# Performance work log

Hardware: AMD Instinct MI355X
Metric: run time of the kernel (lower is better)

The kernel has to match this reference:

```python
import jax, jax.numpy as jnp
import numpy as np

F = 1024
H = 16
DH = F // H  # 64
MLP = 4096
EPS = 1e-5


def layernorm(x, g, b):
    mu = x.mean(-1, keepdims=True)
    var = ((x - mu) ** 2).mean(-1, keepdims=True)
    return (x - mu) * jax.lax.rsqrt(var + EPS) * g + b


def softmax_off_by_one(a):
    e = jnp.exp(a - a.max(-1, keepdims=True))
    return e / (1.0 + e.sum(-1, keepdims=True))


def setup_inputs() -> dict:
    key = jax.random.key(0)
    ks = jax.random.split(key, 12)
    s = 0.02
    return {
        "x": jax.random.normal(ks[0], (2, 2048, F), jnp.float32),
        "ln1_g": jnp.ones((F,), jnp.float32),
        "ln1_b": jnp.zeros((F,), jnp.float32),
        "Wq": jax.random.normal(ks[1], (F, F), jnp.float32) * s,
        "bq": jnp.zeros((F,), jnp.float32),
        "Wk": jax.random.normal(ks[2], (F, F), jnp.float32) * s,
        "bk": jnp.zeros((F,), jnp.float32),
        "Wv": jax.random.normal(ks[3], (F, F), jnp.float32) * s,
        "bv": jnp.zeros((F,), jnp.float32),
        "Wo": jax.random.normal(ks[4], (F, F), jnp.float32) * s,
        "bo": jnp.zeros((F,), jnp.float32),
        "slim": jnp.ones((H,), jnp.float32),
        "ln2_g": jnp.ones((F,), jnp.float32),
        "ln2_b": jnp.zeros((F,), jnp.float32),
        "W1": jax.random.normal(ks[5], (F, MLP), jnp.float32) * s,
        "b1": jnp.zeros((MLP,), jnp.float32),
        "W2": jax.random.normal(ks[6], (MLP, F), jnp.float32) * s,
        "b2": jnp.zeros((F,), jnp.float32),
    }


def reference(x, ln1_g, ln1_b, Wq, bq, Wk, bk, Wv, bv, Wo, bo, slim,
              ln2_g, ln2_b, W1, b1, W2, b2):
    b, n, f = x.shape
    h = layernorm(x, ln1_g, ln1_b)
    # project and split heads: [b, H, n, DH]
    q = (h @ Wq + bq).reshape(b, n, H, DH).transpose(0, 2, 1, 3)
    k = (h @ Wk + bk).reshape(b, n, H, DH).transpose(0, 2, 1, 3)
    v = (h @ Wv + bv).reshape(b, n, H, DH).transpose(0, 2, 1, 3)
    att = jnp.einsum('bhid,bhjd->bhij', q, k) / (DH ** 0.5)
    probs = softmax_off_by_one(att)  # off-by-one softmax
    probs = probs * slim[None, :, None, None]  # slimming after softmax
    attn = jnp.einsum('bhij,bhjd->bihd', probs, v).reshape(b, n, F)
    out = attn @ Wo + bo + x  # residual 1
    h2 = layernorm(out, ln2_g, ln2_b)
    m = jax.nn.gelu(h2 @ W1 + b1, approximate=False)
    m = jax.nn.gelu(m @ W2 + b2, approximate=False)
    return m + out  # residual 2
```

## Files before the change

### kernel.cpp

```cpp
#include <hip/hip_runtime.h>
#include <hip/hip_bf16.h>

typedef __hip_bfloat16 bf16;
typedef short bf16x8 __attribute__((ext_vector_type(8)));
typedef float f32x4 __attribute__((ext_vector_type(4)));

__device__ __forceinline__ float gelu_f(float x) {
  return 0.5f * x * (1.f + erff(x * 0.70710678118654752f));
}

__device__ __forceinline__ unsigned short f2bfu(float f) {
  bf16 h = __float2bfloat16(f);
  unsigned short u;
  __builtin_memcpy(&u, &h, 2);
  return u;
}

__device__ __forceinline__ void load16_lds(const bf16* g, bf16* l) {
  __builtin_amdgcn_global_load_lds(
      (const __attribute__((address_space(1))) unsigned int*)g,
      (__attribute__((address_space(3))) unsigned int*)l, 16, 0, 0);
}

__global__ __launch_bounds__(256) void transpose_cast(
    const float* __restrict__ src, bf16* __restrict__ dst, int R, int C) {
  __shared__ float tile[32][33];
  int tx = threadIdx.x & 31, ty = threadIdx.x >> 5;
  int r0 = blockIdx.y * 32, c0 = blockIdx.x * 32;
  #pragma unroll
  for (int i = ty; i < 32; i += 8)
    tile[i][tx] = src[(size_t)(r0 + i) * C + (c0 + tx)];
  __syncthreads();
  #pragma unroll
  for (int i = ty; i < 32; i += 8)
    dst[(size_t)(c0 + i) * R + (r0 + tx)] = __float2bfloat16(tile[tx][i]);
}

__global__ __launch_bounds__(256) void ln_kernel(
    const float* __restrict__ x, const float* __restrict__ g,
    const float* __restrict__ b, bf16* __restrict__ y) {
  int row = blockIdx.x;
  int t = threadIdx.x;
  const float4* xr = (const float4*)(x + (size_t)row * 1024);
  float4 v = xr[t];
  float s = v.x + v.y + v.z + v.w;
  float ss = v.x * v.x + v.y * v.y + v.z * v.z + v.w * v.w;
  #pragma unroll
  for (int off = 32; off >= 1; off >>= 1) {
    s += __shfl_xor(s, off);
    ss += __shfl_xor(ss, off);
  }
  __shared__ float red[8];
  int wv = t >> 6;
  if ((t & 63) == 0) { red[wv] = s; red[4 + wv] = ss; }
  __syncthreads();
  float S = red[0] + red[1] + red[2] + red[3];
  float SS = red[4] + red[5] + red[6] + red[7];
  float mu = S * (1.f / 1024.f);
  float var = SS * (1.f / 1024.f) - mu * mu;
  float inv = rsqrtf(var + 1e-5f);
  float4 gv = ((const float4*)g)[t];
  float4 bv = ((const float4*)b)[t];
  ushort4 o;
  o.x = f2bfu((v.x - mu) * inv * gv.x + bv.x);
  o.y = f2bfu((v.y - mu) * inv * gv.y + bv.y);
  o.z = f2bfu((v.z - mu) * inv * gv.z + bv.z);
  o.w = f2bfu((v.w - mu) * inv * gv.w + bv.w);
  ((ushort4*)(y + (size_t)row * 1024))[t] = o;
}

template <int EPI>
__global__ __launch_bounds__(256) void gemm_bf16(
    const bf16* __restrict__ A, const bf16* __restrict__ Bt,
    const float* __restrict__ bias0, const float* __restrict__ bias1,
    const float* __restrict__ bias2, const float* __restrict__ resid,
    void* __restrict__ C0, void* __restrict__ C1, void* __restrict__ C2,
    int M, int N, int K) {
  __shared__ __align__(16) bf16 As[2][128 * 32];
  __shared__ __align__(16) bf16 Bs[2][128 * 32];
  const int t = threadIdx.x, lane = t & 63, w = t >> 6;
  const int wm = (w >> 1) * 64, wn = (w & 1) * 64;
  const int m0 = blockIdx.y * 128, n0 = blockIdx.x * 128;

  const int koff = (EPI == 6) ? (int)blockIdx.z * 1024 : 0;
  const int kc_len = (EPI == 6) ? 1024 : K;

  const int srow = lane >> 2;
  const int sgrp = lane & 3;
  f32x4 acc[4][4] = {};

  const bf16* Abase = A + (size_t)m0 * K + koff;
  const bf16* Bbase = Bt + (size_t)n0 * K + koff;

  auto stage = [&](int buf, int kt) {
    #pragma unroll
    for (int c = 0; c < 2; ++c) {
      int row = w * 32 + c * 16 + srow;
      int sw = (row & 3) ^ ((row >> 2) & 3);
      int gg = sgrp ^ sw;
      const bf16* ga = Abase + (size_t)row * K + kt + gg * 8;
      const bf16* gb = Bbase + (size_t)row * K + kt + gg * 8;
      load16_lds(ga, &As[buf][(w * 32 + c * 16) * 32]);
      load16_lds(gb, &Bs[buf][(w * 32 + c * 16) * 32]);
    }
  };

  const int q8 = (((lane >> 4) ^ (lane & 3) ^ ((lane >> 2) & 3))) * 8;
  const int fr = lane & 15;

  const int nk = kc_len >> 5;
  stage(0, 0);
  for (int i = 0; i < nk; ++i) {
    const int cur = i & 1;
    __syncthreads();
    if (i + 1 < nk) stage(cur ^ 1, (i + 1) << 5);
    bf16x8 af[4], bfr[4];
    #pragma unroll
    for (int mc = 0; mc < 4; ++mc)
      af[mc] = *(const bf16x8*)&As[cur][(wm + mc * 16 + fr) * 32 + q8];
    #pragma unroll
    for (int nc = 0; nc < 4; ++nc)
      bfr[nc] = *(const bf16x8*)&Bs[cur][(wn + nc * 16 + fr) * 32 + q8];
    #pragma unroll
    for (int mc = 0; mc < 4; ++mc)
      #pragma unroll
      for (int nc = 0; nc < 4; ++nc)
        acc[mc][nc] = __builtin_amdgcn_mfma_f32_16x16x32_bf16(
            af[mc], bfr[nc], acc[mc][nc], 0, 0, 0);
  }

  if constexpr (EPI == 0) {
    const int which = n0 >> 10;
    const float* bp = which == 0 ? bias0 : which == 1 ? bias1 : bias2;
    bf16* qk = (bf16*)(which == 0 ? C0 : C1);
    const float qscale = 0.18033688011112042f;
    #pragma unroll
    for (int mc = 0; mc < 4; ++mc) {
      #pragma unroll
      for (int reg = 0; reg < 4; ++reg) {
        int m = m0 + wm + mc * 16 + ((lane >> 4) << 2) + reg;
        int b = m >> 11, tok = m & 2047;
        #pragma unroll
        for (int nc = 0; nc < 4; ++nc) {
          int n = n0 + wn + nc * 16 + (lane & 15);
          int nn = n & 1023, hh = nn >> 6, d = n & 63;
          float val = acc[mc][nc][reg] + bp[nn];
          if (which == 2)
            ((bf16*)C2)[(size_t)((b * 16 + hh) * 64 + d) * 2048 + tok] =
                __float2bfloat16(val);
          else if (which == 0)
            qk[(size_t)((b * 16 + hh) * 2048 + tok) * 64 + d] =
                __float2bfloat16(val * qscale);
          else
            qk[(size_t)((b * 16 + hh) * 2048 + tok) * 64 + d] =
                __float2bfloat16(val);
        }
      }
    }
  } else if constexpr (EPI == 6) {
    bf16* pout = (bf16*)C0 + (size_t)blockIdx.z * M * N;
    #pragma unroll
    for (int mc = 0; mc < 4; ++mc) {
      #pragma unroll
      for (int reg = 0; reg < 4; ++reg) {
        int m = m0 + wm + mc * 16 + ((lane >> 4) << 2) + reg;
        #pragma unroll
        for (int nc = 0; nc < 4; ++nc) {
          int n = n0 + wn + nc * 16 + (lane & 15);
          pout[(size_t)m * N + n] = __float2bfloat16(acc[mc][nc][reg]);
        }
      }
    }
  } else {
    #pragma unroll
    for (int mc = 0; mc < 4; ++mc) {
      #pragma unroll
      for (int reg = 0; reg < 4; ++reg) {
        int m = m0 + wm + mc * 16 + ((lane >> 4) << 2) + reg;
        #pragma unroll
        for (int nc = 0; nc < 4; ++nc) {
          int n = n0 + wn + nc * 16 + (lane & 15);
          float val = acc[mc][nc][reg] + bias0[n];
          size_t idx = (size_t)m * N + n;
          if constexpr (EPI == 3) {
            ((float*)C0)[idx] = val + resid[idx];
          } else if constexpr (EPI == 4) {
            ((bf16*)C0)[idx] = __float2bfloat16(gelu_f(val));
          } else {
            ((float*)C0)[idx] = gelu_f(val) + resid[idx];
          }
        }
      }
    }
  }
}

__global__ __launch_bounds__(256) void reduce_mlp2(
    const bf16* __restrict__ part, const float* __restrict__ b2,
    const float* __restrict__ out1, float* __restrict__ out) {
  const int row = blockIdx.x, t = threadIdx.x;
  const size_t base = (size_t)row * 1024 + t * 4;
  float sum[4] = {0.f, 0.f, 0.f, 0.f};
  #pragma unroll
  for (int kc = 0; kc < 4; ++kc) {
    ushort4 u = *(const ushort4*)(part + (size_t)kc * 4096 * 1024 + base);
    unsigned short us[4] = {u.x, u.y, u.z, u.w};
    #pragma unroll
    for (int j = 0; j < 4; ++j) {
      bf16 h;
      __builtin_memcpy(&h, &us[j], 2);
      sum[j] += __bfloat162float(h);
    }
  }
  float4 bv = ((const float4*)b2)[t];
  float4 rv = *(const float4*)(out1 + base);
  float4 o;
  o.x = gelu_f(sum[0] + bv.x) + rv.x;
  o.y = gelu_f(sum[1] + bv.y) + rv.y;
  o.z = gelu_f(sum[2] + bv.z) + rv.z;
  o.w = gelu_f(sum[3] + bv.w) + rv.w;
  *(float4*)(out + base) = o;
}

__global__ __launch_bounds__(256) void attn_kernel(
    const bf16* __restrict__ q, const bf16* __restrict__ k,
    const bf16* __restrict__ vt, const float* __restrict__ slim,
    bf16* __restrict__ attn) {
  __shared__ __align__(16) bf16 Ks[2][64][64];
  __shared__ __align__(16) bf16 Vs[2][64][64];
  __shared__ __align__(16) bf16 Ps[4][16][72];

  const int t = threadIdx.x, lane = t & 63, w = t >> 6;
  const int fr = lane & 15, qd = lane >> 4;
  const int bh = blockIdx.y;
  const int q0 = blockIdx.x * 64;
  const size_t bhbase = (size_t)bh * 2048 * 64;

  const int qrow = q0 + w * 16 + fr;
  const bf16* qp = q + bhbase + (size_t)qrow * 64 + qd * 8;
  bf16x8 qf0 = *(const bf16x8*)qp;
  bf16x8 qf1 = *(const bf16x8*)(qp + 32);

  const int srow = lane >> 3;
  const int sg = lane & 7;

  f32x4 o_acc[4] = {};
  float m_lane[4] = {0.f, 0.f, 0.f, 0.f};
  float l_lane[4] = {0.f, 0.f, 0.f, 0.f};

  auto stage = [&](int buf, int j0) {
    #pragma unroll
    for (int c = 0; c < 2; ++c) {
      int r = w * 16 + c * 8 + srow;
      int gk = sg ^ (r & 7);
      load16_lds(k + bhbase + (size_t)(j0 + r) * 64 + gk * 8,
                 &Ks[buf][w * 16 + c * 8][0]);
      load16_lds(vt + bhbase + (size_t)r * 2048 + j0 + gk * 8,
                 &Vs[buf][w * 16 + c * 8][0]);
    }
  };

  stage(0, 0);
  for (int it = 0; it < 32; ++it) {
    const int cur = it & 1;
    __syncthreads();
    if (it + 1 < 32) stage(cur ^ 1, (it + 1) * 64);

    f32x4 z[4];
    #pragma unroll
    for (int nc = 0; nc < 4; ++nc) {
      int kr = nc * 16 + fr;
      bf16x8 kf0 = *(const bf16x8*)&Ks[cur][kr][(qd ^ (kr & 7)) * 8];
      bf16x8 kf1 = *(const bf16x8*)&Ks[cur][kr][((qd + 4) ^ (kr & 7)) * 8];
      f32x4 zz = {};
      zz = __builtin_amdgcn_mfma_f32_16x16x32_bf16(qf0, kf0, zz, 0, 0, 0);
      zz = __builtin_amdgcn_mfma_f32_16x16x32_bf16(qf1, kf1, zz, 0, 0, 0);
      z[nc] = zz;
    }

    #pragma unroll
    for (int nc = 0; nc < 4; ++nc)
      #pragma unroll
      for (int r = 0; r < 4; ++r) {
        float p = exp2f(z[nc][r]);
        l_lane[r] += p;
        m_lane[r] = fmaxf(m_lane[r], p);
        Ps[w][qd * 4 + r][nc * 16 + fr] = __float2bfloat16(p);
      }

    bf16x8 pf0 = *(const bf16x8*)&Ps[w][fr][qd * 8];
    bf16x8 pf1 = *(const bf16x8*)&Ps[w][fr][32 + qd * 8];
    #pragma unroll
    for (int dc = 0; dc < 4; ++dc) {
      int vr = dc * 16 + fr;
      bf16x8 vf0 = *(const bf16x8*)&Vs[cur][vr][(qd ^ (vr & 7)) * 8];
      bf16x8 vf1 = *(const bf16x8*)&Vs[cur][vr][((qd + 4) ^ (vr & 7)) * 8];
      o_acc[dc] = __builtin_amdgcn_mfma_f32_16x16x32_bf16(pf0, vf0, o_acc[dc], 0, 0, 0);
      o_acc[dc] = __builtin_amdgcn_mfma_f32_16x16x32_bf16(pf1, vf1, o_acc[dc], 0, 0, 0);
    }
  }

  #pragma unroll
  for (int off = 1; off <= 8; off <<= 1)
    #pragma unroll
    for (int r = 0; r < 4; ++r) {
      l_lane[r] += __shfl_xor(l_lane[r], off);
      m_lane[r] = fmaxf(m_lane[r], __shfl_xor(m_lane[r], off));
    }

  const int b = bh >> 4, hh = bh & 15;
  const float sl = slim[hh];
  #pragma unroll
  for (int r = 0; r < 4; ++r) {
    float inv = sl / (m_lane[r] + l_lane[r]);
    int mrow = b * 2048 + q0 + w * 16 + qd * 4 + r;
    #pragma unroll
    for (int dc = 0; dc < 4; ++dc) {
      int col = hh * 64 + dc * 16 + fr;
      attn[(size_t)mrow * 1024 + col] = __float2bfloat16(o_acc[dc][r] * inv);
    }
  }
}

extern "C" void kernel_launch(void* const* d_in, const int* in_sizes, int n_in,
                              void* d_out, int out_size, void* d_ws, size_t ws_size,
                              hipStream_t stream) {
  const float* x    = (const float*)d_in[0];
  const float* ln1g = (const float*)d_in[1];
  const float* ln1b = (const float*)d_in[2];
  const float* Wq   = (const float*)d_in[3];
  const float* bq   = (const float*)d_in[4];
  const float* Wk   = (const float*)d_in[5];
  const float* bk   = (const float*)d_in[6];
  const float* Wv   = (const float*)d_in[7];
  const float* bv   = (const float*)d_in[8];
  const float* Wo   = (const float*)d_in[9];
  const float* bo   = (const float*)d_in[10];
  const float* slim = (const float*)d_in[11];
  const float* ln2g = (const float*)d_in[12];
  const float* ln2b = (const float*)d_in[13];
  const float* W1   = (const float*)d_in[14];
  const float* b1   = (const float*)d_in[15];
  const float* W2   = (const float*)d_in[16];
  const float* b2   = (const float*)d_in[17];

  char* p = (char*)d_ws;
  auto take = [&](size_t nbytes) {
    char* r = p;
    p += (nbytes + 255) & ~(size_t)255;
    return r;
  };
  bf16* Wqkv_t = (bf16*)take((size_t)3072 * 1024 * 2);
  bf16* Wo_t = (bf16*)take((size_t)1024 * 1024 * 2);
  bf16* W1_t = (bf16*)take((size_t)4096 * 1024 * 2);
  bf16* W2_t = (bf16*)take((size_t)1024 * 4096 * 2);
  bf16* h1   = (bf16*)take((size_t)4096 * 1024 * 2);
  bf16* qb   = (bf16*)take((size_t)4096 * 1024 * 2);
  bf16* kb   = (bf16*)take((size_t)4096 * 1024 * 2);
  bf16* vtb  = (bf16*)take((size_t)4096 * 1024 * 2);
  bf16* attn = (bf16*)take((size_t)4096 * 1024 * 2);
  float* out1 = (float*)take((size_t)4096 * 1024 * 4);
  bf16* h2   = (bf16*)take((size_t)4096 * 1024 * 2);
  bf16* m1   = (bf16*)take((size_t)4096 * 4096 * 2);

  bf16* parts = h1;

  dim3 blk(256);

  transpose_cast<<<dim3(32, 32), blk, 0, stream>>>(Wq, Wqkv_t, 1024, 1024);
  transpose_cast<<<dim3(32, 32), blk, 0, stream>>>(Wk, Wqkv_t + (size_t)1024 * 1024, 1024, 1024);
  transpose_cast<<<dim3(32, 32), blk, 0, stream>>>(Wv, Wqkv_t + (size_t)2048 * 1024, 1024, 1024);
  transpose_cast<<<dim3(32, 32), blk, 0, stream>>>(Wo, Wo_t, 1024, 1024);
  transpose_cast<<<dim3(128, 32), blk, 0, stream>>>(W1, W1_t, 1024, 4096);
  transpose_cast<<<dim3(32, 128), blk, 0, stream>>>(W2, W2_t, 4096, 1024);

  ln_kernel<<<4096, blk, 0, stream>>>(x, ln1g, ln1b, h1);

  gemm_bf16<0><<<dim3(24, 32), blk, 0, stream>>>(
      h1, Wqkv_t, bq, bk, bv, nullptr, qb, kb, vtb, 4096, 3072, 1024);

  attn_kernel<<<dim3(32, 32), blk, 0, stream>>>(qb, kb, vtb, slim, attn);

  gemm_bf16<3><<<dim3(8, 32), blk, 0, stream>>>(
      attn, Wo_t, bo, nullptr, nullptr, x, out1, nullptr, nullptr, 4096, 1024, 1024);

  ln_kernel<<<4096, blk, 0, stream>>>(out1, ln2g, ln2b, h2);

  gemm_bf16<4><<<dim3(32, 32), blk, 0, stream>>>(
      h2, W1_t, b1, nullptr, nullptr, nullptr, m1, nullptr, nullptr, 4096, 4096, 1024);

  gemm_bf16<6><<<dim3(8, 32, 4), blk, 0, stream>>>(
      m1, W2_t, nullptr, nullptr, nullptr, nullptr, parts, nullptr, nullptr,
      4096, 1024, 4096);
  reduce_mlp2<<<4096, blk, 0, stream>>>(parts, b2, out1, (float*)d_out);
}
```

Baseline: 468.1 us.

## Stage attention K/V tiles through registers into single padded LDS buffer

Replaces the double-buffered direct global-to-LDS async loads in the attention kernel with register prefetch of the next K/V tile, followed by a store into one padded (stride 72) LDS buffer. The XOR swizzle is replaced by row padding to avoid bank conflicts. The aim is to cut LDS footprint so more blocks fit per CU, and to drop the swizzle index arithmetic. In exchange it adds a second barrier per iteration, extra register use, and LDS store instructions.

Result: faster. 435.3 us (-7.0%).

```diff
diff --git a/kernel.cpp b/kernel.cpp
--- a/kernel.cpp
+++ b/kernel.cpp
@@ -226,8 +226,8 @@
     const bf16* __restrict__ q, const bf16* __restrict__ k,
     const bf16* __restrict__ vt, const float* __restrict__ slim,
     bf16* __restrict__ attn) {
-  __shared__ __align__(16) bf16 Ks[2][64][64];
-  __shared__ __align__(16) bf16 Vs[2][64][64];
+  __shared__ __align__(16) bf16 Ks[64][72];
+  __shared__ __align__(16) bf16 Vs[64][72];
   __shared__ __align__(16) bf16 Ps[4][16][72];
 
   const int t = threadIdx.x, lane = t & 63, w = t >> 6;
@@ -241,37 +241,37 @@
   bf16x8 qf0 = *(const bf16x8*)qp;
   bf16x8 qf1 = *(const bf16x8*)(qp + 32);
 
-  const int srow = lane >> 3;
-  const int sg = lane & 7;
+  const int r0 = t >> 3, g0 = t & 7;
+  const bf16* kbase = k + bhbase + (size_t)r0 * 64 + g0 * 8;
+  const bf16* vbase = vt + bhbase + (size_t)r0 * 2048 + g0 * 8;
+
+  bf16x8 kreg0, kreg1, vreg0, vreg1;
+  auto gload = [&](int j0) {
+    kreg0 = *(const bf16x8*)(kbase + (size_t)j0 * 64);
+    kreg1 = *(const bf16x8*)(kbase + (size_t)(j0 + 32) * 64);
+    vreg0 = *(const bf16x8*)(vbase + j0);
+    vreg1 = *(const bf16x8*)(vbase + (size_t)32 * 2048 + j0);
+  };
+  gload(0);
 
   f32x4 o_acc[4] = {};
   float m_lane[4] = {0.f, 0.f, 0.f, 0.f};
   float l_lane[4] = {0.f, 0.f, 0.f, 0.f};
 
-  auto stage = [&](int buf, int j0) {
-    #pragma unroll
-    for (int c = 0; c < 2; ++c) {
-      int r = w * 16 + c * 8 + srow;
-      int gk = sg ^ (r & 7);
-      load16_lds(k + bhbase + (size_t)(j0 + r) * 64 + gk * 8,
-                 &Ks[buf][w * 16 + c * 8][0]);
-      load16_lds(vt + bhbase + (size_t)r * 2048 + j0 + gk * 8,
-                 &Vs[buf][w * 16 + c * 8][0]);
-    }
-  };
-
-  stage(0, 0);
   for (int it = 0; it < 32; ++it) {
-    const int cur = it & 1;
+    *(bf16x8*)&Ks[r0][g0 * 8] = kreg0;
+    *(bf16x8*)&Ks[r0 + 32][g0 * 8] = kreg1;
+    *(bf16x8*)&Vs[r0][g0 * 8] = vreg0;
+    *(bf16x8*)&Vs[r0 + 32][g0 * 8] = vreg1;
     __syncthreads();
-    if (it + 1 < 32) stage(cur ^ 1, (it + 1) * 64);
+    if (it + 1 < 32) gload((it + 1) * 64);
 
     f32x4 z[4];
     #pragma unroll
     for (int nc = 0; nc < 4; ++nc) {
       int kr = nc * 16 + fr;
-      bf16x8 kf0 = *(const bf16x8*)&Ks[cur][kr][(qd ^ (kr & 7)) * 8];
-      bf16x8 kf1 = *(const bf16x8*)&Ks[cur][kr][((qd + 4) ^ (kr & 7)) * 8];
+      bf16x8 kf0 = *(const bf16x8*)&Ks[kr][qd * 8];
+      bf16x8 kf1 = *(const bf16x8*)&Ks[kr][32 + qd * 8];
       f32x4 zz = {};
       zz = __builtin_amdgcn_mfma_f32_16x16x32_bf16(qf0, kf0, zz, 0, 0, 0);
       zz = __builtin_amdgcn_mfma_f32_16x16x32_bf16(qf1, kf1, zz, 0, 0, 0);
@@ -293,11 +293,12 @@
     #pragma unroll
     for (int dc = 0; dc < 4; ++dc) {
       int vr = dc * 16 + fr;
-      bf16x8 vf0 = *(const bf16x8*)&Vs[cur][vr][(qd ^ (vr & 7)) * 8];
-      bf16x8 vf1 = *(const bf16x8*)&Vs[cur][vr][((qd + 4) ^ (vr & 7)) * 8];
+      bf16x8 vf0 = *(const bf16x8*)&Vs[vr][qd * 8];
+      bf16x8 vf1 = *(const bf16x8*)&Vs[vr][32 + qd * 8];
       o_acc[dc] = __builtin_amdgcn_mfma_f32_16x16x32_bf16(pf0, vf0, o_acc[dc], 0, 0, 0);
       o_acc[dc] = __builtin_amdgcn_mfma_f32_16x16x32_bf16(pf1, vf1, o_acc[dc], 0, 0, 0);
     }
+    __syncthreads();
   }
 
   #pragma unroll
```
